# Optimization experiments

Measured on AMD Instinct MI355X. Metric: run time of the kernel, lower is better.

Reference implementation:

```python
import jax, jax.numpy as jnp
import numpy as np

B, N, CIN, CV, D, H, HD, W, SHIFT = 1024, 192, 63, 27, 256, 8, 32, 8, 4
DEPTH, MLP = 2, 256  # mlp_dim = int(embed_dim * mlp_ratio) = 256


def setup_inputs() -> dict:
    key = jax.random.key(0)
    ks = iter(jax.random.split(key, 64))
    def w(*shape):
        return jax.random.normal(next(ks), shape, jnp.float32) * 0.02
    z = lambda *s: jnp.zeros(s, jnp.float32)
    o = lambda *s: jnp.ones(s, jnp.float32)
    return {
        'input_pts': jax.random.normal(next(ks), (B, N, CIN), jnp.float32),
        'input_views': jax.random.normal(next(ks), (B, CV), jnp.float32),
        'w_in': w(CIN, D), 'b_in': z(D),
        'ln_in_s': o(D), 'ln_in_b': z(D),
        'ln1_s': o(DEPTH, D), 'ln1_b': z(DEPTH, D),
        'wq': w(DEPTH, D, H, HD), 'bq': z(DEPTH, H, HD),
        'wk': w(DEPTH, D, H, HD), 'bk': z(DEPTH, H, HD),
        'wv': w(DEPTH, D, H, HD), 'bv': z(DEPTH, H, HD),
        'wo': w(DEPTH, H, HD, D), 'bo': z(DEPTH, D),
        'ln2_s': o(DEPTH, D), 'ln2_b': z(DEPTH, D),
        'w_mlp1': w(DEPTH, D, MLP), 'b_mlp1': z(DEPTH, MLP),
        'w_mlp2': w(DEPTH, MLP, D), 'b_mlp2': z(DEPTH, D),
        'w_skip': w(DEPTH, CIN + D, D), 'b_skip': z(DEPTH, D),
        'ln_f_s': o(D), 'ln_f_b': z(D),
        'w_alpha': w(D, 1), 'b_alpha': z(1),
        'w_feat': w(D, D), 'b_feat': z(D),
        'w_rgb1': w(D + CV, D // 2), 'b_rgb1': z(D // 2),
        'w_rgb2': w(D // 2, 3), 'b_rgb2': z(3),
    }


def _ln(x, s, b, eps=1e-6):
    m = jnp.mean(x, -1, keepdims=True)
    v = jnp.mean(jnp.square(x - m), -1, keepdims=True)
    return (x - m) * jax.lax.rsqrt(v + eps) * s + b


def _pos_embed(n, d):
    pos = jnp.arange(n, dtype=jnp.float32)[:, None]
    i = jnp.arange(d)
    ang = pos / jnp.power(10000.0, (2 * (i // 2)).astype(jnp.float32) / d)
    return jnp.where(i % 2 == 0, jnp.sin(ang), jnp.cos(ang))[None]  # [1, n, d]


def _block(x, shifted, ln1_s, ln1_b, wq, bq, wk, bk, wv, bv, wo, bo,
           ln2_s, ln2_b, w1, b1, w2, b2):
    b, n, c = x.shape
    y = _ln(x, ln1_s, ln1_b)
    if shifted:
        y = jnp.roll(y, -SHIFT, axis=1)
    yw = y.reshape(b * (n // W), W, c)  # window partition
    q = jnp.einsum('bnc,chd->bnhd', yw, wq) + bq
    k = jnp.einsum('bnc,chd->bnhd', yw, wk) + bk
    v = jnp.einsum('bnc,chd->bnhd', yw, wv) + bv
    scale = np.float32(1.0 / np.sqrt(HD))
    a = jax.nn.softmax(jnp.einsum('bqhd,bkhd->bhqk', q * scale, k), axis=-1)
    o = jnp.einsum('bhqk,bkhd->bqhd', a, v)
    o = jnp.einsum('bqhd,hdc->bqc', o, wo) + bo
    o = o.reshape(b, n, c)  # window reverse
    if shifted:
        o = jnp.roll(o, SHIFT, axis=1)
    x = x + o
    y = _ln(x, ln2_s, ln2_b)
    y = jax.nn.gelu(jnp.einsum('bnc,cm->bnm', y, w1) + b1)
    y = jnp.einsum('bnm,mc->bnc', y, w2) + b2
    return x + y


def reference(input_pts, input_views, w_in, b_in, ln_in_s, ln_in_b,
              ln1_s, ln1_b, wq, bq, wk, bk, wv, bv, wo, bo, ln2_s, ln2_b,
              w_mlp1, b_mlp1, w_mlp2, b_mlp2, w_skip, b_skip,
              ln_f_s, ln_f_b, w_alpha, b_alpha, w_feat, b_feat,
              w_rgb1, b_rgb1, w_rgb2, b_rgb2):
    x = input_pts @ w_in + b_in
    x = _ln(x, ln_in_s, ln_in_b)
    x = x + _pos_embed(x.shape[1], x.shape[2])
    for i in range(DEPTH):  # shift on odd layers; skips = [0, 1]
        x = _block(x, i % 2 == 1, ln1_s[i], ln1_b[i], wq[i], bq[i], wk[i], bk[i],
                   wv[i], bv[i], wo[i], bo[i], ln2_s[i], ln2_b[i],
                   w_mlp1[i], b_mlp1[i], w_mlp2[i], b_mlp2[i])
        x = jax.nn.gelu(jnp.concatenate([input_pts, x], -1) @ w_skip[i] + b_skip[i])
    h = _ln(x, ln_f_s, ln_f_b)
    alpha = h @ w_alpha + b_alpha
    feature = h @ w_feat + b_feat
    views = jnp.repeat(input_views[:, None, :], h.shape[1], axis=1)
    hr = jnp.concatenate([feature, views], -1)
    rgb = jax.nn.gelu(hr @ w_rgb1 + b_rgb1) @ w_rgb2 + b_rgb2
    return rgb, alpha
```

## Files before the change

### kernel.cpp

```cpp
#include <hip/hip_runtime.h>
#include <hip/hip_bf16.h>
#include <math.h>

typedef __hip_bfloat16 bf16;
typedef __attribute__((ext_vector_type(8))) short short8;
typedef __attribute__((ext_vector_type(4))) float f32x4;

#define T_TOK 196608
#define NSEQ  192
#define DMODEL 256
#define CHUNKS 4
#define CHUNKM (T_TOK/CHUNKS)

__device__ __forceinline__ float cvt(float v){ return v; }
__device__ __forceinline__ float cvt(bf16 v){ return __bfloat162float(v); }
__device__ __forceinline__ short bfbits(float f){
  bf16 h = __float2bfloat16(f); return *reinterpret_cast<short*>(&h);
}
__device__ __forceinline__ float bfu(unsigned short v){ return __uint_as_float(((unsigned)v) << 16); }

__device__ __forceinline__ float gelu_f(float x){
  const float k0 = 0.7978845608028654f;
  float u = k0*(x + 0.044715f*x*x*x);
  return x / (1.f + __expf(-2.f*u));
}

__device__ __forceinline__ void barrier_lgkm(){
  asm volatile("s_waitcnt lgkmcnt(0)" ::: "memory");
  __builtin_amdgcn_s_barrier();
  asm volatile("" ::: "memory");
}

__global__ __launch_bounds__(256) void pe_kernel(float* __restrict__ PE){
  int n = blockIdx.x, d = threadIdx.x;
  float e = (float)(2*(d>>1)) / 256.f;
  float ang = (float)n * powf(10000.f, -e);
  PE[n*DMODEL + d] = (d & 1) ? cosf(ang) : sinf(ang);
}

__global__ __launch_bounds__(256) void w2b_kernel(
    const float* __restrict__ src, bf16* __restrict__ dst,
    int K, int N, int KL, int dstStride, int kOff, const float* __restrict__ scale)
{
  int idx = blockIdx.x*256 + threadIdx.x;
  if (idx >= N*KL) return;
  int n = idx / KL, k = idx - n*KL;
  float v = 0.f;
  if (k < K){
    v = src[(size_t)k*N + n];
    if (scale) v *= scale[k];
  }
  dst[(size_t)n*dstStride + kOff + k] = __float2bfloat16(v);
}

__global__ __launch_bounds__(256) void ucalc_kernel(
    const float* __restrict__ W, const float* __restrict__ lnS,
    const float* __restrict__ lnB, const float* __restrict__ bias,
    float* __restrict__ u, float* __restrict__ wB, int K, int N)
{
  __shared__ float pu[4], pb[4];
  const int n = blockIdx.x;
  const int k = threadIdx.x;
  float su = 0.f, sb = 0.f;
  if (k < K){
    float w = W[(size_t)k*N + n];
    su = cvt(__float2bfloat16(lnS[k]*w));
    sb = lnB[k]*w;
  }
  #pragma unroll
  for (int off = 32; off; off >>= 1){
    su += __shfl_xor(su, off, 64);
    sb += __shfl_xor(sb, off, 64);
  }
  int lane = k & 63, wv = k >> 6;
  if (lane == 0){ pu[wv] = su; pb[wv] = sb; }
  __syncthreads();
  if (k == 0){
    u[n]  = pu[0]+pu[1]+pu[2]+pu[3];
    wB[n] = pb[0]+pb[1]+pb[2]+pb[3] + bias[n];
  }
}

__global__ __launch_bounds__(256) void pts2b_kernel(
    const float* __restrict__ src, bf16* __restrict__ dst)
{
  int idx = blockIdx.x*256 + threadIdx.x;
  int t = idx >> 6, k = idx & 63;
  dst[idx] = __float2bfloat16(k < 63 ? src[(size_t)t*63 + k] : 0.f);
}

__global__ __launch_bounds__(256) void views2b_kernel(
    const float* __restrict__ src, bf16* __restrict__ dst)
{
  int idx = blockIdx.x*256 + threadIdx.x;
  int t = idx >> 5, k = idx & 31;
  dst[idx] = __float2bfloat16(k < 27 ? src[(size_t)t*27 + k] : 0.f);
}

__global__ __launch_bounds__(256) void ln_pe_kernel(
    bf16* __restrict__ X, const float* __restrict__ s, const float* __restrict__ b,
    const float* __restrict__ PE, float* __restrict__ s1o, float* __restrict__ s2o)
{
  const int lane = threadIdx.x & 63, w = threadIdx.x >> 6;
  const size_t t = (size_t)blockIdx.x * 4 + w;
  const int n = (int)(t % NSEQ);
  const int c = lane * 4;

  ushort4 u = *reinterpret_cast<const ushort4*>(X + t*DMODEL + c);
  float x0 = bfu(u.x), x1 = bfu(u.y), x2 = bfu(u.z), x3 = bfu(u.w);

  float sx = x0 + x1 + x2 + x3;
  float sq = x0*x0 + x1*x1 + x2*x2 + x3*x3;
  #pragma unroll
  for (int off = 32; off; off >>= 1){
    sx += __shfl_xor(sx, off, 64);
    sq += __shfl_xor(sq, off, 64);
  }
  float mean = sx * (1.f/256.f);
  float var  = sq * (1.f/256.f) - mean*mean;
  float rstd = rsqrtf(var + 1e-6f);

  float4 sv = *reinterpret_cast<const float4*>(s + c);
  float4 bv = *reinterpret_cast<const float4*>(b + c);
  float4 pv = *reinterpret_cast<const float4*>(PE + n*DMODEL + c);

  float y0 = (x0 - mean)*rstd*sv.x + bv.x + pv.x;
  float y1 = (x1 - mean)*rstd*sv.y + bv.y + pv.y;
  float y2 = (x2 - mean)*rstd*sv.z + bv.z + pv.z;
  float y3 = (x3 - mean)*rstd*sv.w + bv.w + pv.w;

  ushort4 o;
  o.x = (unsigned short)bfbits(y0);
  o.y = (unsigned short)bfbits(y1);
  o.z = (unsigned short)bfbits(y2);
  o.w = (unsigned short)bfbits(y3);
  *reinterpret_cast<ushort4*>(X + t*DMODEL + c) = o;

  float sy  = y0 + y1 + y2 + y3;
  float syq = y0*y0 + y1*y1 + y2*y2 + y3*y3;
  #pragma unroll
  for (int off = 32; off; off >>= 1){
    sy  += __shfl_xor(sy,  off, 64);
    syq += __shfl_xor(syq, off, 64);
  }
  if (lane == 0){ s1o[t] = sy; s2o[t] = syq; }
}

template<int MODE, bool LNF, bool ADD, bool GELU, bool STATS>
__global__ __launch_bounds__(256) void gemm_mfma(
    const bf16* __restrict__ A1, int lda1,
    const bf16* __restrict__ A2, int lda2, int SB, int aOff,
    const float* __restrict__ s1i, const float* __restrict__ s2i,
    const float* __restrict__ uvec,
    const bf16* __restrict__ WT, int Kpad, const float* __restrict__ bias,
    bf16* __restrict__ C, int ldc, size_t segStride, int cOff, int rollShift,
    float* __restrict__ s1o, float* __restrict__ s2o)
{
  __shared__ short buf[17408];
  short* As0 = buf;
  short* As1 = buf + 5120;
  short* Cs  = buf;
  __shared__ float sScale[128], sAlpha[128];

  const int tid = threadIdx.x;
  const int lane = tid & 63, wid = tid >> 6;
  const int wm = wid >> 1, wn = wid & 1;
  const int col16 = lane & 15, quad = lane >> 4;
  const int sm = tid >> 1, half = tid & 1;
  const int m0 = blockIdx.y * 128, n0 = blockIdx.x * 128;

  f32x4 acc[4][4];
  #pragma unroll
  for (int i = 0; i < 4; i++)
    #pragma unroll
    for (int j = 0; j < 4; j++) acc[i][j] = (f32x4){0.f,0.f,0.f,0.f};

  int row = m0 + sm;
  if (MODE == 0 && rollShift){
    int bb = row / NSEQ;
    int n  = row - bb*NSEQ;
    n += rollShift; if (n >= NSEQ) n -= NSEQ;
    row = bb*NSEQ + n;
  }
  const size_t arow = (size_t)aOff + row;
  const size_t arow2 = (MODE == 3) ? (arow / NSEQ) : arow;

  if (LNF && tid < 128){
    int r2 = m0 + tid;
    if (rollShift){
      int bb = r2 / NSEQ, n = r2 - bb*NSEQ;
      n += rollShift; if (n >= NSEQ) n -= NSEQ;
      r2 = bb*NSEQ + n;
    }
    size_t r = (size_t)aOff + r2;
    float m1 = s1i[r] * (1.f/256.f);
    float m2 = s2i[r] * (1.f/256.f);
    float rs = rsqrtf(m2 - m1*m1 + 1e-6f);
    sScale[tid] = rs;
    sAlpha[tid] = -m1*rs;
  }

  auto loadA = [&](int k0, uint4& u0, uint4& u1){
    const int gk = k0 + half*16;
    const bf16* src;
    if (MODE == 0) src = A1 + arow*(size_t)lda1 + gk;
    else src = (gk < SB) ? (A1 + arow*(size_t)lda1 + gk)
                         : (A2 + arow2*(size_t)lda2 + (gk - SB));
    u0 = *(const uint4*)(src);
    u1 = *(const uint4*)(src + 8);
  };
  auto writeA = [&](short* dst, const uint4& u0, const uint4& u1){
    *(uint4*)&dst[sm*40 + half*16]     = u0;
    *(uint4*)&dst[sm*40 + half*16 + 8] = u1;
  };

  uint4 p0, p1;
  loadA(0, p0, p1);
  writeA(As0, p0, p1);
  if (Kpad > 32) loadA(32, p0, p1);
  barrier_lgkm();

  int cur = 0;
  for (int k0 = 0; k0 < Kpad; k0 += 32){
    const short* Asc = cur ? As1 : As0;
    short8 afr[4];
    #pragma unroll
    for (int mi = 0; mi < 4; mi++)
      afr[mi] = *(const short8*)&Asc[(wm*64 + mi*16 + col16)*40 + quad*8];
    short8 bfr[4];
    #pragma unroll
    for (int ni = 0; ni < 4; ni++)
      bfr[ni] = *(const short8*)((const short*)WT
                 + (size_t)(n0 + wn*64 + ni*16 + col16)*Kpad + k0 + quad*8);
    #pragma unroll
    for (int mi = 0; mi < 4; mi++)
      #pragma unroll
      for (int ni = 0; ni < 4; ni++)
        acc[mi][ni] = __builtin_amdgcn_mfma_f32_16x16x32_bf16(
            afr[mi], bfr[ni], acc[mi][ni], 0, 0, 0);
    if (k0 + 32 < Kpad){
      short* Asn = cur ? As0 : As1;
      writeA(Asn, p0, p1);
      if (k0 + 64 < Kpad) loadA(k0+64, p0, p1);
    }
    barrier_lgkm();
    cur ^= 1;
  }

  #pragma unroll
  for (int ni = 0; ni < 4; ni++){
    int ncol = wn*64 + ni*16 + col16;
    float bv = bias[n0 + ncol];
    float uv = LNF ? uvec[n0 + ncol] : 0.f;
    #pragma unroll
    for (int mi = 0; mi < 4; mi++){
      f32x4 a = acc[mi][ni];
      #pragma unroll
      for (int r = 0; r < 4; r++){
        int lrow = wm*64 + mi*16 + quad*4 + r;
        float val;
        if (LNF) val = sScale[lrow]*a[r] + sAlpha[lrow]*uv + bv;
        else     val = a[r] + bv;
        if (GELU) val = gelu_f(val);
        Cs[lrow*136 + ncol] = bfbits(val);
      }
    }
  }
  __syncthreads();

  const int seg = n0 >> 8;
  const int nb  = n0 & 255;
  const int orow = tid >> 4;
  const int ocol = (tid & 15) * 8;
  #pragma unroll
  for (int p = 0; p < 8; p++){
    int lrow = p*16 + orow;
    size_t mrow = (size_t)cOff + m0 + lrow;
    short8 v = *(const short8*)&Cs[lrow*136 + ocol];
    bf16* dst = C + (size_t)seg*segStride + mrow*ldc + nb + ocol;
    float rowSum = 0.f, rowSq = 0.f;
    if (ADD){
      short8 c = *(const short8*)dst;
      short8 o;
      #pragma unroll
      for (int e = 0; e < 8; e++){
        bf16 va, ca;
        *reinterpret_cast<short*>(&va) = v[e];
        *reinterpret_cast<short*>(&ca) = c[e];
        float f = cvt(va) + cvt(ca);
        o[e] = bfbits(f);
        if (STATS){ rowSum += f; rowSq += f*f; }
      }
      *(short8*)dst = o;
    } else {
      if (STATS){
        #pragma unroll
        for (int e = 0; e < 8; e++){
          bf16 va; *reinterpret_cast<short*>(&va) = v[e];
          float f = cvt(va);
          rowSum += f; rowSq += f*f;
        }
      }
      *(short8*)dst = v;
    }
    if (STATS){
      #pragma unroll
      for (int mk = 1; mk <= 8; mk <<= 1){
        rowSum += __shfl_xor(rowSum, mk, 64);
        rowSq  += __shfl_xor(rowSq,  mk, 64);
      }
      if ((tid & 15) == 0){
        atomicAdd(&s1o[mrow], rowSum);
        atomicAdd(&s2o[mrow], rowSq);
      }
    }
  }
}

__global__ __launch_bounds__(256) void mlp_skip_fused(
    const bf16* __restrict__ X,
    const bf16* __restrict__ PTS,
    const float* __restrict__ s1i, const float* __restrict__ s2i,
    const float* __restrict__ uvec,
    const bf16* __restrict__ W1T,
    const float* __restrict__ wB1,
    const bf16* __restrict__ W2T,
    const float* __restrict__ b2,
    const bf16* __restrict__ WSK,
    const float* __restrict__ bsk,
    bf16* __restrict__ Z,
    float* __restrict__ s1o, float* __restrict__ s2o)
{
  __shared__ short sT[64*264];
  short* As0 = sT;
  short* As1 = sT + 2560;
  short* Cs  = sT;
  __shared__ float sScale[64], sAlpha[64];

  const int tid = threadIdx.x;
  const int lane = tid & 63, wid = tid >> 6;
  const int col16 = lane & 15, quad = lane >> 4;
  const int qr = tid >> 2, qc = tid & 3;
  const int m0 = blockIdx.x * 64;
  const int orow = tid >> 5;
  const int oc   = (tid & 31) * 8;

  if (tid < 64){
    size_t r = (size_t)m0 + tid;
    float m1 = s1i[r] * (1.f/256.f);
    float m2 = s2i[r] * (1.f/256.f);
    float rs = rsqrtf(m2 - m1*m1 + 1e-6f);
    sScale[tid] = rs;
    sAlpha[tid] = -m1*rs;
  }

  const size_t arow = (size_t)m0 + qr;
  auto loadA = [&](int k0, uint4& u){
    u = *(const uint4*)(X + arow*DMODEL + k0 + qc*8);
  };
  auto writeA = [&](short* dst, const uint4& u){
    *(uint4*)&dst[qr*40 + qc*8] = u;
  };

  f32x4 acc[4][4];
  #pragma unroll
  for (int i = 0; i < 4; i++)
    #pragma unroll
    for (int j = 0; j < 4; j++) acc[i][j] = (f32x4){0.f,0.f,0.f,0.f};

  uint4 p;
  loadA(0, p); writeA(As0, p);
  loadA(32, p);
  barrier_lgkm();
  int cur = 0;
  for (int k0 = 0; k0 < 256; k0 += 32){
    const short* Asc = cur ? As1 : As0;
    short8 afr[4];
    #pragma unroll
    for (int mi = 0; mi < 4; mi++)
      afr[mi] = *(const short8*)&Asc[(mi*16 + col16)*40 + quad*8];
    short8 bfr[4];
    #pragma unroll
    for (int ni = 0; ni < 4; ni++)
      bfr[ni] = *(const short8*)((const short*)W1T
                 + (size_t)(wid*64 + ni*16 + col16)*256 + k0 + quad*8);
    #pragma unroll
    for (int mi = 0; mi < 4; mi++)
      #pragma unroll
      for (int ni = 0; ni < 4; ni++)
        acc[mi][ni] = __builtin_amdgcn_mfma_f32_16x16x32_bf16(
            afr[mi], bfr[ni], acc[mi][ni], 0, 0, 0);
    if (k0 + 32 < 256){
      short* Asn = cur ? As0 : As1;
      writeA(Asn, p);
      if (k0 + 64 < 256) loadA(k0 + 64, p);
    }
    barrier_lgkm();
    cur ^= 1;
  }

  #pragma unroll
  for (int ni = 0; ni < 4; ni++){
    int ncol = wid*64 + ni*16 + col16;
    float uv = uvec[ncol];
    float bv = wB1[ncol];
    #pragma unroll
    for (int mi = 0; mi < 4; mi++){
      f32x4 a = acc[mi][ni];
      #pragma unroll
      for (int r = 0; r < 4; r++){
        int lrow = mi*16 + quad*4 + r;
        float val = sScale[lrow]*a[r] + sAlpha[lrow]*uv + bv;
        sT[lrow*264 + ncol] = bfbits(gelu_f(val));
      }
    }
  }
  __syncthreads();

  f32x4 acc2[4][4];
  #pragma unroll
  for (int i = 0; i < 4; i++)
    #pragma unroll
    for (int j = 0; j < 4; j++) acc2[i][j] = (f32x4){0.f,0.f,0.f,0.f};
  for (int k0 = 0; k0 < 256; k0 += 32){
    short8 afr[4];
    #pragma unroll
    for (int mi = 0; mi < 4; mi++)
      afr[mi] = *(const short8*)&sT[(mi*16 + col16)*264 + k0 + quad*8];
    short8 bfr[4];
    #pragma unroll
    for (int ni = 0; ni < 4; ni++)
      bfr[ni] = *(const short8*)((const short*)W2T
                 + (size_t)(wid*64 + ni*16 + col16)*256 + k0 + quad*8);
    #pragma unroll
    for (int mi = 0; mi < 4; mi++)
      #pragma unroll
      for (int ni = 0; ni < 4; ni++)
        acc2[mi][ni] = __builtin_amdgcn_mfma_f32_16x16x32_bf16(
            afr[mi], bfr[ni], acc2[mi][ni], 0, 0, 0);
  }
  __syncthreads();

  #pragma unroll
  for (int ni = 0; ni < 4; ni++){
    int ncol = wid*64 + ni*16 + col16;
    float bv = b2[ncol];
    #pragma unroll
    for (int mi = 0; mi < 4; mi++){
      f32x4 a = acc2[mi][ni];
      #pragma unroll
      for (int r = 0; r < 4; r++){
        int lrow = mi*16 + quad*4 + r;
        sT[lrow*264 + ncol] = bfbits(a[r] + bv);
      }
    }
  }
  __syncthreads();

  #pragma unroll
  for (int pp = 0; pp < 8; pp++){
    int lrow = pp*8 + orow;
    short8 xv = *(const short8*)(X + ((size_t)m0 + lrow)*DMODEL + oc);
    short8 tv = *(const short8*)&sT[lrow*264 + oc];
    short8 o;
    #pragma unroll
    for (int e = 0; e < 8; e++)
      o[e] = bfbits(bfu((unsigned short)xv[e]) + bfu((unsigned short)tv[e]));
    *(short8*)&sT[lrow*264 + oc] = o;
  }
  __syncthreads();

  const bf16* pp4[4];
  #pragma unroll
  for (int mi = 0; mi < 4; mi++)
    pp4[mi] = PTS + (size_t)(m0 + mi*16 + col16)*64 + quad*8;

  f32x4 acc3[4][4];
  #pragma unroll
  for (int i = 0; i < 4; i++)
    #pragma unroll
    for (int j = 0; j < 4; j++) acc3[i][j] = (f32x4){0.f,0.f,0.f,0.f};
  for (int k0 = 0; k0 < 320; k0 += 32){
    short8 afr[4];
    if (k0 < 64){
      #pragma unroll
      for (int mi = 0; mi < 4; mi++)
        afr[mi] = *(const short8*)(pp4[mi] + k0);
    } else {
      #pragma unroll
      for (int mi = 0; mi < 4; mi++)
        afr[mi] = *(const short8*)&sT[(mi*16 + col16)*264 + (k0 - 64) + quad*8];
    }
    short8 bfr[4];
    #pragma unroll
    for (int ni = 0; ni < 4; ni++)
      bfr[ni] = *(const short8*)((const short*)WSK
                 + (size_t)(wid*64 + ni*16 + col16)*320 + k0 + quad*8);
    #pragma unroll
    for (int mi = 0; mi < 4; mi++)
      #pragma unroll
      for (int ni = 0; ni < 4; ni++)
        acc3[mi][ni] = __builtin_amdgcn_mfma_f32_16x16x32_bf16(
            afr[mi], bfr[ni], acc3[mi][ni], 0, 0, 0);
  }
  __syncthreads();

  #pragma unroll
  for (int ni = 0; ni < 4; ni++){
    int ncol = wid*64 + ni*16 + col16;
    float bv = bsk[ncol];
    #pragma unroll
    for (int mi = 0; mi < 4; mi++){
      f32x4 a = acc3[mi][ni];
      #pragma unroll
      for (int r = 0; r < 4; r++){
        int lrow = mi*16 + quad*4 + r;
        Cs[lrow*264 + ncol] = bfbits(gelu_f(a[r] + bv));
      }
    }
  }
  __syncthreads();

  #pragma unroll
  for (int pp = 0; pp < 8; pp++){
    int lrow = pp*8 + orow;
    size_t mrow = (size_t)m0 + lrow;
    short8 v = *(const short8*)&Cs[lrow*264 + oc];
    float rowSum = 0.f, rowSq = 0.f;
    #pragma unroll
    for (int e = 0; e < 8; e++){
      float f = bfu((unsigned short)v[e]);
      rowSum += f; rowSq += f*f;
    }
    *(short8*)(Z + mrow*DMODEL + oc) = v;
    #pragma unroll
    for (int mk = 1; mk <= 16; mk <<= 1){
      rowSum += __shfl_xor(rowSum, mk, 64);
      rowSq  += __shfl_xor(rowSq,  mk, 64);
    }
    if ((tid & 31) == 0){
      s1o[mrow] = rowSum;
      s2o[mrow] = rowSq;
    }
  }
}

__global__ __launch_bounds__(256) void attn_lite(
    bf16* __restrict__ Qg, const bf16* __restrict__ Kg, const bf16* __restrict__ Vg)
{
  __shared__ short Qs[16*264], Ks[16*264], Vs[16*264];
  __shared__ float sc[2*8*8*8];
  const int tid = threadIdx.x;
  const size_t base = (size_t)blockIdx.x * 16 * 256;

  #pragma unroll
  for (int it = 0; it < 2; it++){
    int c = it*256 + tid;
    int row = c >> 5, cb = (c & 31) * 8;
    size_t g = base + (size_t)row*256 + cb;
    *(uint4*)&Qs[row*264 + cb] = *(const uint4*)(Qg + g);
    *(uint4*)&Ks[row*264 + cb] = *(const uint4*)(Kg + g);
    *(uint4*)&Vs[row*264 + cb] = *(const uint4*)(Vg + g);
  }
  __syncthreads();

  const float scale = 0.17677669529663687f;
  if (tid < 128){
    int win = tid >> 6, h = (tid >> 3) & 7, qi = tid & 7;
    int qrow = win*8 + qi;
    short8 qv[4];
    #pragma unroll
    for (int j = 0; j < 4; j++)
      qv[j] = *(const short8*)&Qs[qrow*264 + h*32 + j*8];
    float s[8];
    #pragma unroll
    for (int k = 0; k < 8; k++){
      int krow = win*8 + k;
      float a = 0.f;
      #pragma unroll
      for (int j = 0; j < 4; j++){
        short8 kv = *(const short8*)&Ks[krow*264 + h*32 + j*8];
        #pragma unroll
        for (int e = 0; e < 8; e++)
          a += bfu((unsigned short)qv[j][e]) * bfu((unsigned short)kv[e]);
      }
      s[k] = a * scale;
    }
    float mx = s[0];
    #pragma unroll
    for (int k = 1; k < 8; k++) mx = fmaxf(mx, s[k]);
    float sum = 0.f;
    #pragma unroll
    for (int k = 0; k < 8; k++){ s[k] = __expf(s[k] - mx); sum += s[k]; }
    float inv = 1.f / sum;
    #pragma unroll
    for (int k = 0; k < 8; k++)
      sc[((win*8 + qi)*8 + h)*8 + k] = s[k] * inv;
  }
  __syncthreads();

  {
    const int c = tid, h = c >> 5;
    #pragma unroll
    for (int j = 0; j < 16; j++){
      int win = j >> 3, qi = j & 7;
      const float* pr = &sc[((win*8 + qi)*8 + h)*8];
      float o = 0.f;
      #pragma unroll
      for (int k = 0; k < 8; k++)
        o += pr[k] * bfu((unsigned short)Vs[(win*8 + k)*264 + c]);
      Qs[j*264 + c] = bfbits(o);
    }
  }
  __syncthreads();

  #pragma unroll
  for (int it = 0; it < 2; it++){
    int c = it*256 + tid;
    int row = c >> 5, cb = (c & 31) * 8;
    *(uint4*)(Qg + base + (size_t)row*256 + cb) = *(uint4*)&Qs[row*264 + cb];
  }
}

__global__ __launch_bounds__(256) void alpha_kernel(
    const bf16* __restrict__ X, const float* __restrict__ s1,
    const float* __restrict__ s2, const float* __restrict__ s,
    const float* __restrict__ b, const float* __restrict__ wa,
    const float* __restrict__ ba, float* __restrict__ out)
{
  int lane = threadIdx.x & 63, w = threadIdx.x >> 6;
  size_t t = (size_t)blockIdx.x * 4 + w;
  float m = s1[t] * (1.f/256.f);
  float q = s2[t] * (1.f/256.f);
  float r = rsqrtf(q - m*m + 1e-6f);
  float acc = 0.f;
  #pragma unroll
  for (int j = 0; j < 4; j++){
    int c = lane + 64*j;
    float y = (cvt(X[t*DMODEL + c]) - m) * r * s[c] + b[c];
    acc += y * wa[c];
  }
  #pragma unroll
  for (int off = 32; off; off >>= 1) acc += __shfl_down(acc, off, 64);
  if (lane == 0) out[t] = acc + ba[0];
}

__global__ __launch_bounds__(256) void rgb2_kernel(
    const bf16* __restrict__ T1, const float* __restrict__ w2,
    const float* __restrict__ b2, float* __restrict__ out)
{
  int lane = threadIdx.x & 63, w = threadIdx.x >> 6;
  size_t t = (size_t)blockIdx.x * 4 + w;
  float h0 = cvt(T1[t*256 + lane]);
  float h1 = cvt(T1[t*256 + 64 + lane]);
  float a0 = h0*w2[lane*3+0] + h1*w2[(lane+64)*3+0];
  float a1 = h0*w2[lane*3+1] + h1*w2[(lane+64)*3+1];
  float a2 = h0*w2[lane*3+2] + h1*w2[(lane+64)*3+2];
  #pragma unroll
  for (int off = 32; off; off >>= 1){
    a0 += __shfl_down(a0, off, 64);
    a1 += __shfl_down(a1, off, 64);
    a2 += __shfl_down(a2, off, 64);
  }
  if (lane == 0){
    out[t*3+0] = a0 + b2[0];
    out[t*3+1] = a1 + b2[1];
    out[t*3+2] = a2 + b2[2];
  }
}

extern "C" void kernel_launch(void* const* d_in, const int* in_sizes, int n_in,
                              void* d_out, int out_size, void* d_ws, size_t ws_size,
                              hipStream_t stream)
{
  (void)in_sizes; (void)n_in; (void)out_size;
  const float* pts     = (const float*)d_in[0];
  const float* views   = (const float*)d_in[1];
  const float* w_in    = (const float*)d_in[2];
  const float* b_in    = (const float*)d_in[3];
  const float* ln_in_s = (const float*)d_in[4];
  const float* ln_in_b = (const float*)d_in[5];
  const float* ln1_s   = (const float*)d_in[6];
  const float* ln1_b   = (const float*)d_in[7];
  const float* wq      = (const float*)d_in[8];
  const float* bq      = (const float*)d_in[9];
  const float* wk      = (const float*)d_in[10];
  const float* bk      = (const float*)d_in[11];
  const float* wv      = (const float*)d_in[12];
  const float* bv      = (const float*)d_in[13];
  const float* wo      = (const float*)d_in[14];
  const float* bo      = (const float*)d_in[15];
  const float* ln2_s   = (const float*)d_in[16];
  const float* ln2_b   = (const float*)d_in[17];
  const float* w_mlp1  = (const float*)d_in[18];
  const float* b_mlp1  = (const float*)d_in[19];
  const float* w_mlp2  = (const float*)d_in[20];
  const float* b_mlp2  = (const float*)d_in[21];
  const float* w_skip  = (const float*)d_in[22];
  const float* b_skip  = (const float*)d_in[23];
  const float* ln_f_s  = (const float*)d_in[24];
  const float* ln_f_b  = (const float*)d_in[25];
  const float* w_alpha = (const float*)d_in[26];
  const float* b_alpha = (const float*)d_in[27];
  const float* w_feat  = (const float*)d_in[28];
  const float* b_feat  = (const float*)d_in[29];
  const float* w_rgb1  = (const float*)d_in[30];
  const float* b_rgb1  = (const float*)d_in[31];
  const float* w_rgb2  = (const float*)d_in[32];
  const float* b_rgb2  = (const float*)d_in[33];

  const size_t SZ = (size_t)T_TOK * DMODEL * 2;
  const size_t WT_ELEMS = 16384 + 2*(196608 + 3*65536 + 81920) + 65536 + 36864;
  const size_t UV_FLOATS = 2*768*2 + 2*256*2 + 2*256;
  const size_t NEED = 2*SZ + (size_t)4*T_TOK*4 + NSEQ*DMODEL*4 + UV_FLOATS*4
                    + WT_ELEMS*2 + (size_t)T_TOK*64*2 + 1024*32*2;
  if (ws_size < NEED) return;

  char* wsp = (char*)d_ws;
  bf16* xr = (bf16*)(wsp);
  bf16* x2 = (bf16*)(wsp + SZ);
  float* s1A = (float*)(wsp + 2*SZ);
  float* s2A = s1A + T_TOK;
  float* s1B = s2A + T_TOK;
  float* s2B = s1B + T_TOK;
  float* PE  = s2B + T_TOK;
  float* uvp = PE + NSEQ*DMODEL;
  float* uqkv[2], *wBqkv[2], *um1[2], *wBm1[2];
  {
    float* q = uvp;
    for (int i = 0; i < 2; i++){ uqkv[i] = q; q += 768; }
    for (int i = 0; i < 2; i++){ wBqkv[i] = q; q += 768; }
    for (int i = 0; i < 2; i++){ um1[i] = q; q += 256; }
    for (int i = 0; i < 2; i++){ wBm1[i] = q; q += 256; }
  }
  float* ufeat  = uvp + 2*768*2 + 2*256*2;
  float* wBfeat = ufeat + 256;
  bf16* wtp = (bf16*)(uvp + UV_FLOATS);

  bf16* wt_in = wtp;
  bf16* wt_qkv[2], *wt_o[2], *wt_m1[2], *wt_m2[2], *wt_sk[2];
  bf16* p = wt_in + 16384;
  for (int i = 0; i < 2; i++){
    wt_qkv[i] = p; p += 196608;
    wt_o[i]   = p; p += 65536;
    wt_m1[i]  = p; p += 65536;
    wt_m2[i]  = p; p += 65536;
    wt_sk[i]  = p; p += 81920;
  }
  bf16* wt_feat = p; p += 65536;
  bf16* wt_rgb1 = p; p += 36864;
  bf16* pts_b   = p; p += (size_t)T_TOK*64;
  bf16* views_b = p; p += 1024*32;

  float* out_rgb   = (float*)d_out;
  float* out_alpha = out_rgb + (size_t)T_TOK * 3;

  dim3 blk(256);
  dim3 g256(2, T_TOK/128);
  dim3 gQKV(6, CHUNKM/128);
  dim3 gC(2, CHUNKM/128);
  dim3 g128(1, T_TOK/128);
  dim3 gLN(T_TOK/4);
  dim3 gMLP(T_TOK/64);
  dim3 gStat(T_TOK/4);
  dim3 gAttn(CHUNKM/16);

  const float* NF = nullptr;
  const bf16*  NB = nullptr;
  float* NFW = nullptr;

  pe_kernel<<<dim3(NSEQ), blk, 0, stream>>>(PE);
  pts2b_kernel<<<dim3(T_TOK*64/256), blk, 0, stream>>>(pts, pts_b);
  views2b_kernel<<<dim3(1024*32/256), blk, 0, stream>>>(views, views_b);
  #define W2B(src, dst, K_, N_, KL_, ST_, KO_, SC_) \
    w2b_kernel<<<dim3(((N_)*(KL_)+255)/256), blk, 0, stream>>>(src, dst, K_, N_, KL_, ST_, KO_, SC_)
  W2B(w_in, wt_in, 63, 256, 64, 64, 0, NF);
  for (int i = 0; i < 2; i++){
    const float* s1 = ln1_s + i*256;
    const float* b1 = ln1_b + i*256;
    W2B(wq + (size_t)i*65536, wt_qkv[i],            256, 256, 256, 256, 0, s1);
    W2B(wk + (size_t)i*65536, wt_qkv[i] + 65536,    256, 256, 256, 256, 0, s1);
    W2B(wv + (size_t)i*65536, wt_qkv[i] + 131072,   256, 256, 256, 256, 0, s1);
    ucalc_kernel<<<dim3(256), blk, 0, stream>>>(wq + (size_t)i*65536, s1, b1,
        bq + i*256, uqkv[i],       wBqkv[i],       256, 256);
    ucalc_kernel<<<dim3(256), blk, 0, stream>>>(wk + (size_t)i*65536, s1, b1,
        bk + i*256, uqkv[i] + 256, wBqkv[i] + 256, 256, 256);
    ucalc_kernel<<<dim3(256), blk, 0, stream>>>(wv + (size_t)i*65536, s1, b1,
        bv + i*256, uqkv[i] + 512, wBqkv[i] + 512, 256, 256);
    W2B(wo + (size_t)i*65536, wt_o[i],  256, 256, 256, 256, 0, NF);
    W2B(w_mlp1 + (size_t)i*65536, wt_m1[i], 256, 256, 256, 256, 0, ln2_s + i*256);
    ucalc_kernel<<<dim3(256), blk, 0, stream>>>(w_mlp1 + (size_t)i*65536,
        ln2_s + i*256, ln2_b + i*256, b_mlp1 + i*256, um1[i], wBm1[i], 256, 256);
    W2B(w_mlp2 + (size_t)i*65536, wt_m2[i], 256, 256, 256, 256, 0, NF);
    W2B(w_skip + (size_t)i*81664,            wt_sk[i], 63, 256, 64, 320, 0, NF);
    W2B(w_skip + (size_t)i*81664 + 63*256,   wt_sk[i], 256, 256, 256, 320, 64, NF);
  }
  W2B(w_feat, wt_feat, 256, 256, 256, 256, 0, ln_f_s);
  ucalc_kernel<<<dim3(256), blk, 0, stream>>>(w_feat, ln_f_s, ln_f_b, b_feat,
      ufeat, wBfeat, 256, 256);
  W2B(w_rgb1,                wt_rgb1, 256, 128, 256, 288, 0, NF);
  W2B(w_rgb1 + 256*128,      wt_rgb1, 27, 128, 32, 288, 256, NF);
  #undef W2B

  gemm_mfma<0,false,false,false,false><<<g256, blk, 0, stream>>>(pts_b, 64,
      NB, 0, 0, 0, NF, NF, NF, wt_in, 64, b_in,
      xr, 256, 0, 0, 0, NFW, NFW);
  ln_pe_kernel<<<gLN, blk, 0, stream>>>(xr, ln_in_s, ln_in_b, PE, s1A, s2A);

  for (int i = 0; i < 2; i++){
    const int shift = (i == 1) ? 4 : 0;
    const int shiftBack = (i == 1) ? (NSEQ - 4) : 0;

    hipMemsetAsync(s1B, 0, (size_t)2*T_TOK*4, stream);

    bf16* qb = x2;
    bf16* kb = x2 + (size_t)CHUNKM * 256;
    bf16* vb = x2 + (size_t)2 * CHUNKM * 256;
    for (int cch = 0; cch < CHUNKS; cch++){
      int base = cch * CHUNKM;
      gemm_mfma<0,true,false,false,false><<<gQKV, blk, 0, stream>>>(xr, 256,
          NB, 0, 0, base, s1A, s2A, uqkv[i], wt_qkv[i], 256, wBqkv[i],
          x2, 256, (size_t)CHUNKM*256, 0, shift, NFW, NFW);
      attn_lite<<<gAttn, blk, 0, stream>>>(qb, kb, vb);
      gemm_mfma<0,false,true,false,true><<<gC, blk, 0, stream>>>(qb, 256,
          NB, 0, 0, 0, NF, NF, NF, wt_o[i], 256, bo + i*256,
          xr, 256, 0, base, shiftBack, s1B, s2B);
    }

    mlp_skip_fused<<<gMLP, blk, 0, stream>>>(xr, pts_b, s1B, s2B, um1[i],
        wt_m1[i], wBm1[i], wt_m2[i], b_mlp2 + i*256,
        wt_sk[i], b_skip + i*256, x2, s1A, s2A);
    bf16* tmp = xr; xr = x2; x2 = tmp;
  }

  alpha_kernel<<<gStat, blk, 0, stream>>>(xr, s1A, s2A, ln_f_s, ln_f_b,
      w_alpha, b_alpha, out_alpha);
  gemm_mfma<0,true,false,false,false><<<g256, blk, 0, stream>>>(xr, 256,
      NB, 0, 0, 0, s1A, s2A, ufeat, wt_feat, 256, wBfeat,
      x2, 256, 0, 0, 0, NFW, NFW);
  gemm_mfma<3,false,false,true,false><<<g128, blk, 0, stream>>>(x2, 256,
      views_b, 32, 256, 0, NF, NF, NF, wt_rgb1, 288, b_rgb1,
      xr, 256, 0, 0, 0, NFW, NFW);
  rgb2_kernel<<<gStat, blk, 0, stream>>>(xr, w_rgb2, b_rgb2, out_rgb);
}
```

Measured before the change: 1.869 ms.

## Fuse QKV projection, window attention and output projection into one kernel

Replaces the chunked sequence of QKV GEMM, attention and output-projection kernels with one kernel. Each block handles 16 tokens (two windows): it gathers the shifted rows, computes LN-folded QKV with MFMA into shared memory, runs softmax attention, applies the output projection plus residual, and writes back in place with row statistics. This removes the Q/K/V round trip through global memory, the memset and the per-chunk launches. The cost is that every 16-row block streams the full QKV and O weight matrices straight from global/L2 with no LDS tiling, so weight traffic and MFMA utilisation per block may be poor.

```diff
diff --git a/kernel.cpp b/kernel.cpp
--- a/kernel.cpp
+++ b/kernel.cpp
@@ -9,8 +9,6 @@
 #define T_TOK 196608
 #define NSEQ  192
 #define DMODEL 256
-#define CHUNKS 4
-#define CHUNKM (T_TOK/CHUNKS)
 
 __device__ __forceinline__ float cvt(float v){ return v; }
 __device__ __forceinline__ float cvt(bf16 v){ return __bfloat162float(v); }
@@ -317,6 +315,186 @@
   }
 }
 
+__global__ __launch_bounds__(256) void attn_layer_fused(
+    bf16* __restrict__ X,
+    const float* __restrict__ s1i, const float* __restrict__ s2i,
+    const float* __restrict__ uq,
+    const bf16* __restrict__ WQKV,
+    const float* __restrict__ wBq,
+    const bf16* __restrict__ WO,
+    const float* __restrict__ bov,
+    float* __restrict__ s1o, float* __restrict__ s2o,
+    int shift)
+{
+  __shared__ short xs[16*264];
+  __shared__ short Qs[16*264], Ks[16*264], Vs[16*264];
+  __shared__ float sc[2*8*8*8];
+  __shared__ float sScale[16], sAlpha[16];
+  __shared__ int   srcRow[16];
+
+  const int tid = threadIdx.x;
+  const int lane = tid & 63, wid = tid >> 6;
+  const int col16 = lane & 15, quad = lane >> 4;
+  const int m0 = blockIdx.x * 16;
+
+  if (tid < 16){
+    int row = m0 + tid;
+    int bb = row / NSEQ, n = row - bb*NSEQ;
+    n += shift; if (n >= NSEQ) n -= NSEQ;
+    int src = bb*NSEQ + n;
+    srcRow[tid] = src;
+    float m1 = s1i[src] * (1.f/256.f);
+    float m2 = s2i[src] * (1.f/256.f);
+    float rs = rsqrtf(m2 - m1*m1 + 1e-6f);
+    sScale[tid] = rs;
+    sAlpha[tid] = -m1*rs;
+  }
+  __syncthreads();
+
+  #pragma unroll
+  for (int it = 0; it < 2; it++){
+    int c = it*256 + tid;
+    int row = c >> 5, cb = (c & 31) * 8;
+    *(uint4*)&xs[row*264 + cb] =
+        *(const uint4*)(X + (size_t)srcRow[row]*DMODEL + cb);
+  }
+  __syncthreads();
+
+  {
+    short* dstSeg[3] = {Qs, Ks, Vs};
+    #pragma unroll
+    for (int seg = 0; seg < 3; seg++){
+      f32x4 acc[4];
+      #pragma unroll
+      for (int j = 0; j < 4; j++) acc[j] = (f32x4){0.f,0.f,0.f,0.f};
+      for (int k0 = 0; k0 < 256; k0 += 32){
+        short8 afr = *(const short8*)&xs[col16*264 + k0 + quad*8];
+        #pragma unroll
+        for (int ni = 0; ni < 4; ni++){
+          short8 bfr = *(const short8*)((const short*)WQKV
+              + (size_t)(seg*256 + wid*64 + ni*16 + col16)*256 + k0 + quad*8);
+          acc[ni] = __builtin_amdgcn_mfma_f32_16x16x32_bf16(
+              afr, bfr, acc[ni], 0, 0, 0);
+        }
+      }
+      #pragma unroll
+      for (int ni = 0; ni < 4; ni++){
+        int ncol = wid*64 + ni*16 + col16;
+        float uv = uq[seg*256 + ncol];
+        float bv = wBq[seg*256 + ncol];
+        #pragma unroll
+        for (int r = 0; r < 4; r++){
+          int lrow = quad*4 + r;
+          float val = sScale[lrow]*acc[ni][r] + sAlpha[lrow]*uv + bv;
+          dstSeg[seg][lrow*264 + ncol] = bfbits(val);
+        }
+      }
+    }
+  }
+  __syncthreads();
+
+  const float scale = 0.17677669529663687f;
+  if (tid < 128){
+    int win = tid >> 6, h = (tid >> 3) & 7, qi = tid & 7;
+    int qrow = win*8 + qi;
+    short8 qv[4];
+    #pragma unroll
+    for (int j = 0; j < 4; j++)
+      qv[j] = *(const short8*)&Qs[qrow*264 + h*32 + j*8];
+    float s[8];
+    #pragma unroll
+    for (int k = 0; k < 8; k++){
+      int krow = win*8 + k;
+      float a = 0.f;
+      #pragma unroll
+      for (int j = 0; j < 4; j++){
+        short8 kv = *(const short8*)&Ks[krow*264 + h*32 + j*8];
+        #pragma unroll
+        for (int e = 0; e < 8; e++)
+          a += bfu((unsigned short)qv[j][e]) * bfu((unsigned short)kv[e]);
+      }
+      s[k] = a * scale;
+    }
+    float mx = s[0];
+    #pragma unroll
+    for (int k = 1; k < 8; k++) mx = fmaxf(mx, s[k]);
+    float sum = 0.f;
+    #pragma unroll
+    for (int k = 0; k < 8; k++){ s[k] = __expf(s[k] - mx); sum += s[k]; }
+    float inv = 1.f / sum;
+    #pragma unroll
+    for (int k = 0; k < 8; k++)
+      sc[((win*8 + qi)*8 + h)*8 + k] = s[k] * inv;
+  }
+  __syncthreads();
+
+  {
+    const int c = tid, h = c >> 5;
+    #pragma unroll
+    for (int j = 0; j < 16; j++){
+      int win = j >> 3, qi = j & 7;
+      const float* pr = &sc[((win*8 + qi)*8 + h)*8];
+      float o = 0.f;
+      #pragma unroll
+      for (int k = 0; k < 8; k++)
+        o += pr[k] * bfu((unsigned short)Vs[(win*8 + k)*264 + c]);
+      Qs[j*264 + c] = bfbits(o);
+    }
+  }
+  __syncthreads();
+
+  f32x4 acc2[4];
+  #pragma unroll
+  for (int j = 0; j < 4; j++) acc2[j] = (f32x4){0.f,0.f,0.f,0.f};
+  for (int k0 = 0; k0 < 256; k0 += 32){
+    short8 afr = *(const short8*)&Qs[col16*264 + k0 + quad*8];
+    #pragma unroll
+    for (int ni = 0; ni < 4; ni++){
+      short8 bfr = *(const short8*)((const short*)WO
+          + (size_t)(wid*64 + ni*16 + col16)*256 + k0 + quad*8);
+      acc2[ni] = __builtin_amdgcn_mfma_f32_16x16x32_bf16(
+          afr, bfr, acc2[ni], 0, 0, 0);
+    }
+  }
+  __syncthreads();
+
+  #pragma unroll
+  for (int ni = 0; ni < 4; ni++){
+    int ncol = wid*64 + ni*16 + col16;
+    float bv = bov[ncol];
+    #pragma unroll
+    for (int r = 0; r < 4; r++){
+      int lrow = quad*4 + r;
+      float xv = bfu((unsigned short)xs[lrow*264 + ncol]);
+      Ks[lrow*264 + ncol] = bfbits(acc2[ni][r] + bv + xv);
+    }
+  }
+  __syncthreads();
+
+  #pragma unroll
+  for (int it = 0; it < 2; it++){
+    int c = it*256 + tid;
+    int row = c >> 5, cb = (c & 31) * 8;
+    short8 v = *(const short8*)&Ks[row*264 + cb];
+    float rowSum = 0.f, rowSq = 0.f;
+    #pragma unroll
+    for (int e = 0; e < 8; e++){
+      float f = bfu((unsigned short)v[e]);
+      rowSum += f; rowSq += f*f;
+    }
+    *(uint4*)(X + (size_t)srcRow[row]*DMODEL + cb) = *(uint4*)&v;
+    #pragma unroll
+    for (int mk = 1; mk <= 16; mk <<= 1){
+      rowSum += __shfl_xor(rowSum, mk, 64);
+      rowSq  += __shfl_xor(rowSq,  mk, 64);
+    }
+    if ((tid & 31) == 0){
+      s1o[srcRow[row]] = rowSum;
+      s2o[srcRow[row]] = rowSq;
+    }
+  }
+}
+
 __global__ __launch_bounds__(256) void mlp_skip_fused(
     const bf16* __restrict__ X,
     const bf16* __restrict__ PTS,
@@ -542,83 +720,6 @@
       s1o[mrow] = rowSum;
       s2o[mrow] = rowSq;
     }
-  }
-}
-
-__global__ __launch_bounds__(256) void attn_lite(
-    bf16* __restrict__ Qg, const bf16* __restrict__ Kg, const bf16* __restrict__ Vg)
-{
-  __shared__ short Qs[16*264], Ks[16*264], Vs[16*264];
-  __shared__ float sc[2*8*8*8];
-  const int tid = threadIdx.x;
-  const size_t base = (size_t)blockIdx.x * 16 * 256;
-
-  #pragma unroll
-  for (int it = 0; it < 2; it++){
-    int c = it*256 + tid;
-    int row = c >> 5, cb = (c & 31) * 8;
-    size_t g = base + (size_t)row*256 + cb;
-    *(uint4*)&Qs[row*264 + cb] = *(const uint4*)(Qg + g);
-    *(uint4*)&Ks[row*264 + cb] = *(const uint4*)(Kg + g);
-    *(uint4*)&Vs[row*264 + cb] = *(const uint4*)(Vg + g);
-  }
-  __syncthreads();
-
-  const float scale = 0.17677669529663687f;
-  if (tid < 128){
-    int win = tid >> 6, h = (tid >> 3) & 7, qi = tid & 7;
-    int qrow = win*8 + qi;
-    short8 qv[4];
-    #pragma unroll
-    for (int j = 0; j < 4; j++)
-      qv[j] = *(const short8*)&Qs[qrow*264 + h*32 + j*8];
-    float s[8];
-    #pragma unroll
-    for (int k = 0; k < 8; k++){
-      int krow = win*8 + k;
-      float a = 0.f;
-      #pragma unroll
-      for (int j = 0; j < 4; j++){
-        short8 kv = *(const short8*)&Ks[krow*264 + h*32 + j*8];
-        #pragma unroll
-        for (int e = 0; e < 8; e++)
-          a += bfu((unsigned short)qv[j][e]) * bfu((unsigned short)kv[e]);
-      }
-      s[k] = a * scale;
-    }
-    float mx = s[0];
-    #pragma unroll
-    for (int k = 1; k < 8; k++) mx = fmaxf(mx, s[k]);
-    float sum = 0.f;
-    #pragma unroll
-    for (int k = 0; k < 8; k++){ s[k] = __expf(s[k] - mx); sum += s[k]; }
-    float inv = 1.f / sum;
-    #pragma unroll
-    for (int k = 0; k < 8; k++)
-      sc[((win*8 + qi)*8 + h)*8 + k] = s[k] * inv;
-  }
-  __syncthreads();
-
-  {
-    const int c = tid, h = c >> 5;
-    #pragma unroll
-    for (int j = 0; j < 16; j++){
-      int win = j >> 3, qi = j & 7;
-      const float* pr = &sc[((win*8 + qi)*8 + h)*8];
-      float o = 0.f;
-      #pragma unroll
-      for (int k = 0; k < 8; k++)
-        o += pr[k] * bfu((unsigned short)Vs[(win*8 + k)*264 + c]);
-      Qs[j*264 + c] = bfbits(o);
-    }
-  }
-  __syncthreads();
-
-  #pragma unroll
-  for (int it = 0; it < 2; it++){
-    int c = it*256 + tid;
-    int row = c >> 5, cb = (c & 31) * 8;
-    *(uint4*)(Qg + base + (size_t)row*256 + cb) = *(uint4*)&Qs[row*264 + cb];
   }
 }
 
@@ -757,13 +858,11 @@
 
   dim3 blk(256);
   dim3 g256(2, T_TOK/128);
-  dim3 gQKV(6, CHUNKM/128);
-  dim3 gC(2, CHUNKM/128);
   dim3 g128(1, T_TOK/128);
   dim3 gLN(T_TOK/4);
   dim3 gMLP(T_TOK/64);
+  dim3 gATT(T_TOK/16);
   dim3 gStat(T_TOK/4);
-  dim3 gAttn(CHUNKM/16);
 
   const float* NF = nullptr;
   const bf16*  NB = nullptr;
@@ -809,23 +908,9 @@
 
   for (int i = 0; i < 2; i++){
     const int shift = (i == 1) ? 4 : 0;
-    const int shiftBack = (i == 1) ? (NSEQ - 4) : 0;
-
-    hipMemsetAsync(s1B, 0, (size_t)2*T_TOK*4, stream);
-
-    bf16* qb = x2;
-    bf16* kb = x2 + (size_t)CHUNKM * 256;
-    bf16* vb = x2 + (size_t)2 * CHUNKM * 256;
-    for (int cch = 0; cch < CHUNKS; cch++){
-      int base = cch * CHUNKM;
-      gemm_mfma<0,true,false,false,false><<<gQKV, blk, 0, stream>>>(xr, 256,
-          NB, 0, 0, base, s1A, s2A, uqkv[i], wt_qkv[i], 256, wBqkv[i],
-          x2, 256, (size_t)CHUNKM*256, 0, shift, NFW, NFW);
-      attn_lite<<<gAttn, blk, 0, stream>>>(qb, kb, vb);
-      gemm_mfma<0,false,true,false,true><<<gC, blk, 0, stream>>>(qb, 256,
-          NB, 0, 0, 0, NF, NF, NF, wt_o[i], 256, bo + i*256,
-          xr, 256, 0, base, shiftBack, s1B, s2B);
-    }
+
+    attn_layer_fused<<<gATT, blk, 0, stream>>>(xr, s1A, s2A,
+        uqkv[i], wt_qkv[i], wBqkv[i], wt_o[i], bo + i*256, s1B, s2B, shift);
 
     mlp_skip_fused<<<gMLP, blk, 0, stream>>>(xr, pts_b, s1B, s2B, um1[i],
         wt_m1[i], wBm1[i], wt_m2[i], b_mlp2 + i*256,
```

Result: slower. 2.380 ms (+27.3%).
